# Kernel tuning notes

Measured on AMD Instinct MI355X. Metric: run time of the kernel, lower is better.

The kernel has to match this reference:

```python
import jax, jax.numpy as jnp
import numpy as np

NUM_EXPERTS = 8
TOP_K = 2
RANK = 16
LORA_ALPHA = 32
SCALING = LORA_ALPHA / RANK  # 2.0


def setup_inputs() -> dict:
    key = jax.random.key(0)
    ks = jax.random.split(key, 6)
    B, S, D_IN, D_OUT = 4, 2048, 4096, 4096
    x = jax.random.normal(ks[0], (B, S, D_IN), dtype=jnp.float32)
    W_base = jax.random.normal(ks[1], (D_OUT, D_IN), dtype=jnp.float32) * 0.02
    b_base = jax.random.normal(ks[2], (D_OUT,), dtype=jnp.float32) * 0.02
    W_router = jax.random.normal(ks[3], (NUM_EXPERTS, D_IN), dtype=jnp.float32) * 0.02
    A = jax.random.normal(ks[4], (NUM_EXPERTS, RANK, D_IN), dtype=jnp.float32) * 0.02
    Bm = jax.random.normal(ks[5], (D_OUT, RANK), dtype=jnp.float32) * 0.02
    Bm = jnp.broadcast_to(Bm, (NUM_EXPERTS, D_OUT, RANK)) * jnp.arange(1, NUM_EXPERTS + 1, dtype=jnp.float32)[:, None, None] * 0.2
    return {"x": x, "W_base": W_base, "b_base": b_base, "W_router": W_router, "A": A, "B": Bm}


def reference(x, W_base, b_base, W_router, A, B):
    bs, seq, d_in = x.shape
    T = bs * seq
    xf = x.reshape(T, d_in)  # flatten tokens, as in torch .view(-1, d_in)

    # base linear layer
    base = xf @ W_base.T + b_base  # [T, d_out]

    # local router: logits -> top-k -> softmax over selected weights
    logits = xf @ W_router.T                      # [T, E]
    rw, sel = jax.lax.top_k(logits, TOP_K)        # [T, K] each
    rw = jax.nn.softmax(rw, axis=-1)              # router_norm == 'softmax'

    # per-token per-expert combine weight (zero for unselected experts);
    # mathematically identical to gather-LoRA-scatter since top-k experts
    # per token are distinct.
    onehot = jax.nn.one_hot(sel, NUM_EXPERTS, dtype=rw.dtype)  # [T, K, E]
    w = jnp.einsum('tk,tke->te', rw, onehot)                   # [T, E]

    # LoRA: down-project to tiny rank, weight, then up-project; contract
    # expert+rank together to avoid a [T, E, d_out] intermediate.
    h = jnp.einsum('td,erd->ter', xf, A)          # [T, E, r] (small)
    lora = jnp.einsum('ter,te,eor->to', h, w, B) * SCALING  # [T, d_out]

    return (base + lora).reshape(bs, seq, -1)
```

## Files before the change

### kernel.cpp

```cpp
#include <hip/hip_runtime.h>
#include <hip/hip_bf16.h>
#include <stdint.h>

#define T_TOKENS 8192
#define DIN      4096
#define DOUT     4096
#define NE       8
#define RANK     16
#define KEXT     128
#define KTOT     4224
#define SCALING  2.0f

typedef __attribute__((ext_vector_type(8))) short   short8;
typedef __attribute__((ext_vector_type(4))) float   float4v;

__device__ __forceinline__ unsigned short f2bf(float f) {
    union { float f; unsigned int u; } c; c.f = f;
    unsigned int u = c.u;
    u += 0x7FFFu + ((u >> 16) & 1u);
    return (unsigned short)(u >> 16);
}

#define GLD_LDS(g, l) __builtin_amdgcn_global_load_lds( \
    (const __attribute__((address_space(1))) void*)(g), \
    (__attribute__((address_space(3))) void*)(l), 16, 0, 0)

__global__ __launch_bounds__(256) void k_prep_w(const float* __restrict__ Wb,
                                                unsigned short* __restrict__ Wa) {
    int idx = blockIdx.x * 256 + threadIdx.x;
    const float4* W4 = (const float4*)Wb;
    float4 v = W4[idx];
    int o  = idx >> 10;
    int kc = idx & 1023;
    ushort4 p;
    p.x = f2bf(v.x); p.y = f2bf(v.y); p.z = f2bf(v.z); p.w = f2bf(v.w);
    *(ushort4*)(Wa + (size_t)o * KTOT + kc * 4) = p;
}

__global__ __launch_bounds__(256) void k_prep_small(const float* __restrict__ A,
                                                    const float* __restrict__ Bm,
                                                    unsigned short* __restrict__ Acat,
                                                    unsigned short* __restrict__ Wa) {
    int tid = blockIdx.x * 256 + threadIdx.x;
    if (tid < NE * RANK * DIN) {
        Acat[tid] = f2bf(A[tid]);
    } else {
        int j   = tid - NE * RANK * DIN;
        int o   = j >> 7;
        int rem = j & 127;
        int e   = rem >> 4;
        int r   = rem & 15;
        Wa[(size_t)o * KTOT + DIN + rem] = f2bf(Bm[(size_t)e * (DOUT * RANK) + o * RANK + r]);
    }
}

__global__ __launch_bounds__(256) void k_router(const float* __restrict__ x,
                                                const float* __restrict__ Wr,
                                                unsigned short* __restrict__ xa,
                                                float* __restrict__ w8) {
    int t   = blockIdx.x;
    int tid = threadIdx.x;
    const float4* x4  = (const float4*)(x + (size_t)t * DIN);
    const float4* Wr4 = (const float4*)Wr;
    unsigned short* xrow = xa + (size_t)t * KTOT;

    float p[NE];
#pragma unroll
    for (int e = 0; e < NE; e++) p[e] = 0.f;

#pragma unroll
    for (int j = 0; j < 4; j++) {
        int c = tid + j * 256;
        float4 v = x4[c];
        ushort4 b;
        b.x = f2bf(v.x); b.y = f2bf(v.y); b.z = f2bf(v.z); b.w = f2bf(v.w);
        *(ushort4*)(xrow + c * 4) = b;
#pragma unroll
        for (int e = 0; e < NE; e++) {
            float4 wv = Wr4[e * 1024 + c];
            p[e] += v.x * wv.x + v.y * wv.y + v.z * wv.z + v.w * wv.w;
        }
    }
#pragma unroll
    for (int e = 0; e < NE; e++) {
        float v = p[e];
#pragma unroll
        for (int off = 32; off > 0; off >>= 1) v += __shfl_xor(v, off);
        p[e] = v;
    }
    __shared__ float red[4][NE];
    int lane = tid & 63, w = tid >> 6;
    if (lane == 0) {
#pragma unroll
        for (int e = 0; e < NE; e++) red[w][e] = p[e];
    }
    __syncthreads();
    if (tid == 0) {
        float lg[NE];
#pragma unroll
        for (int e = 0; e < NE; e++)
            lg[e] = red[0][e] + red[1][e] + red[2][e] + red[3][e];
        int e0 = 0;
#pragma unroll
        for (int e = 1; e < NE; e++) if (lg[e] > lg[e0]) e0 = e;
        int e1 = -1;
#pragma unroll
        for (int e = 0; e < NE; e++)
            if (e != e0 && (e1 < 0 || lg[e] > lg[e1])) e1 = e;
        float a0 = 1.0f;
        float a1 = __expf(lg[e1] - lg[e0]);
        float inv = 1.0f / (a0 + a1);
        float s0 = a0 * inv * SCALING;
        float s1 = a1 * inv * SCALING;
        float* wrow = w8 + t * NE;
#pragma unroll
        for (int e = 0; e < NE; e++)
            wrow[e] = (e == e0) ? s0 : ((e == e1) ? s1 : 0.f);
    }
}

__global__ __launch_bounds__(256) void k_h(unsigned short* xa,
                                           const unsigned short* __restrict__ Acat,
                                           const float* __restrict__ w8) {
    __shared__ unsigned short lds[32 * 32 + 128 * 32];
    int m0  = blockIdx.x * 32;
    int tid = threadIdx.x;
    int l = tid & 63, w = tid >> 6;
    int quad = l >> 4, lr = l & 15;

    float4v acc[2][2] = {};

    for (int k0 = 0; k0 < DIN; k0 += 32) {
        __syncthreads();
        if (w < 2) {
            int c = w * 64 + l;
            int row = c >> 2, kc = c & 3;
            GLD_LDS(xa + (size_t)(m0 + row) * KTOT + k0 + kc * 8, lds + c * 8);
        }
#pragma unroll
        for (int it = 0; it < 2; it++) {
            int c = it * 256 + w * 64 + l;
            int row = c >> 2, kc = c & 3;
            GLD_LDS(Acat + (size_t)row * DIN + k0 + kc * 8, lds + 1024 + c * 8);
        }
        __syncthreads();

        short8 a[2], b[2];
#pragma unroll
        for (int mi = 0; mi < 2; mi++)
            a[mi] = *(const short8*)(lds + (mi * 16 + lr) * 32 + quad * 8);
#pragma unroll
        for (int ni = 0; ni < 2; ni++)
            b[ni] = *(const short8*)(lds + 1024 + (w * 32 + ni * 16 + lr) * 32 + quad * 8);
#pragma unroll
        for (int mi = 0; mi < 2; mi++)
#pragma unroll
            for (int ni = 0; ni < 2; ni++)
                acc[mi][ni] = __builtin_amdgcn_mfma_f32_16x16x32_bf16(a[mi], b[ni], acc[mi][ni], 0, 0, 0);
    }

#pragma unroll
    for (int mi = 0; mi < 2; mi++)
#pragma unroll
        for (int ni = 0; ni < 2; ni++) {
            int col = w * 32 + ni * 16 + lr;
            int e = col >> 4;
#pragma unroll
            for (int i = 0; i < 4; i++) {
                int t = m0 + mi * 16 + quad * 4 + i;
                float v = acc[mi][ni][i] * w8[t * NE + e];
                xa[(size_t)t * KTOT + DIN + col] = f2bf(v);
            }
        }
}

__global__ __launch_bounds__(256) void k_main(const unsigned short* __restrict__ xa,
                                              const unsigned short* __restrict__ Wa,
                                              const float* __restrict__ bias,
                                              float* __restrict__ out) {
    __shared__ unsigned short lds[2 * 128 * 32];
    int bm = blockIdx.x, bn = blockIdx.y;
    int tid = threadIdx.x;
    int l = tid & 63, w = tid >> 6;
    int quad = l >> 4, lr = l & 15;
    int wm = w >> 1, wn = w & 1;

    const size_t xbase = (size_t)bm * 128 * KTOT;
    const size_t wbase = (size_t)bn * 128 * KTOT;

    float4v acc[4][4] = {};

    for (int k0 = 0; k0 < KTOT; k0 += 32) {
        __syncthreads();
#pragma unroll
        for (int it = 0; it < 2; it++) {
            int c = it * 256 + w * 64 + l;
            int row = c >> 2, kc = c & 3;
            GLD_LDS(xa + xbase + (size_t)row * KTOT + k0 + kc * 8, lds + c * 8);
            GLD_LDS(Wa + wbase + (size_t)row * KTOT + k0 + kc * 8, lds + 4096 + c * 8);
        }
        __syncthreads();

        short8 a[4], b[4];
#pragma unroll
        for (int mi = 0; mi < 4; mi++)
            a[mi] = *(const short8*)(lds + (wm * 64 + mi * 16 + lr) * 32 + quad * 8);
#pragma unroll
        for (int ni = 0; ni < 4; ni++)
            b[ni] = *(const short8*)(lds + 4096 + (wn * 64 + ni * 16 + lr) * 32 + quad * 8);
#pragma unroll
        for (int mi = 0; mi < 4; mi++)
#pragma unroll
            for (int ni = 0; ni < 4; ni++)
                acc[mi][ni] = __builtin_amdgcn_mfma_f32_16x16x32_bf16(a[mi], b[ni], acc[mi][ni], 0, 0, 0);
    }

    int trow0 = bm * 128 + wm * 64;
    int ocol0 = bn * 128 + wn * 64;
#pragma unroll
    for (int ni = 0; ni < 4; ni++) {
        int o = ocol0 + ni * 16 + lr;
        float bb = bias[o];
#pragma unroll
        for (int mi = 0; mi < 4; mi++) {
#pragma unroll
            for (int i = 0; i < 4; i++) {
                int t = trow0 + mi * 16 + quad * 4 + i;
                out[(size_t)t * DOUT + o] = acc[mi][ni][i] + bb;
            }
        }
    }
}

extern "C" void kernel_launch(void* const* d_in, const int* in_sizes, int n_in,
                              void* d_out, int out_size, void* d_ws, size_t ws_size,
                              hipStream_t stream) {
    const float* x  = (const float*)d_in[0];
    const float* Wb = (const float*)d_in[1];
    const float* bb = (const float*)d_in[2];
    const float* Wr = (const float*)d_in[3];
    const float* A  = (const float*)d_in[4];
    const float* Bm = (const float*)d_in[5];
    float* out = (float*)d_out;

    char* ws = (char*)d_ws;
    unsigned short* xa   = (unsigned short*)(ws);
    unsigned short* Wa   = (unsigned short*)(ws + 69206016);
    unsigned short* Acat = (unsigned short*)(ws + 69206016 + 34603008);
    float*          w8   = (float*)(ws + 69206016 + 34603008 + 1048576);

    k_prep_w    <<<dim3(16384), dim3(256), 0, stream>>>(Wb, Wa);
    k_prep_small<<<dim3(4096),  dim3(256), 0, stream>>>(A, Bm, Acat, Wa);
    k_router    <<<dim3(8192),  dim3(256), 0, stream>>>(x, Wr, xa, w8);
    k_h         <<<dim3(256),   dim3(256), 0, stream>>>(xa, Acat, w8);
    k_main      <<<dim3(64, 32), dim3(256), 0, stream>>>(xa, Wa, bb, out);
}
```

Before: 707.9 us.

## Fuse router and LoRA down-projection, merge prep kernels, swizzle LDS in main GEMM

Merges the two weight-prep kernels into one launch. Fuses the router logits, x bf16 conversion and the LoRA down-projection into a single 256-block kernel that converts each x row once and reuses it from LDS, instead of re-reading bf16 x from global memory. Adds an XOR swizzle to the LDS layout in the main GEMM and the fused kernel to reduce bank conflicts on the MFMA operand loads. The fused front kernel launches only 256 blocks, so the large fp32 x read is spread over fewer workgroups, which may lower bandwidth utilisation compared with the former 8192-block router.

```diff
diff --git a/kernel.cpp b/kernel.cpp
--- a/kernel.cpp
+++ b/kernel.cpp
@@ -25,81 +25,131 @@
     (const __attribute__((address_space(1))) void*)(g), \
     (__attribute__((address_space(3))) void*)(l), 16, 0, 0)
 
-__global__ __launch_bounds__(256) void k_prep_w(const float* __restrict__ Wb,
-                                                unsigned short* __restrict__ Wa) {
-    int idx = blockIdx.x * 256 + threadIdx.x;
-    const float4* W4 = (const float4*)Wb;
-    float4 v = W4[idx];
-    int o  = idx >> 10;
-    int kc = idx & 1023;
-    ushort4 p;
-    p.x = f2bf(v.x); p.y = f2bf(v.y); p.z = f2bf(v.z); p.w = f2bf(v.w);
-    *(ushort4*)(Wa + (size_t)o * KTOT + kc * 4) = p;
-}
-
-__global__ __launch_bounds__(256) void k_prep_small(const float* __restrict__ A,
-                                                    const float* __restrict__ Bm,
-                                                    unsigned short* __restrict__ Acat,
-                                                    unsigned short* __restrict__ Wa) {
-    int tid = blockIdx.x * 256 + threadIdx.x;
-    if (tid < NE * RANK * DIN) {
-        Acat[tid] = f2bf(A[tid]);
+__global__ __launch_bounds__(256) void k_prep(const float* __restrict__ Wb,
+                                              const float* __restrict__ A,
+                                              const float* __restrict__ Bm,
+                                              unsigned short* __restrict__ Wa,
+                                              unsigned short* __restrict__ Acat) {
+    int b = blockIdx.x;
+    if (b < 16384) {
+        int idx = b * 256 + threadIdx.x;
+        const float4* W4 = (const float4*)Wb;
+        float4 v = W4[idx];
+        int o  = idx >> 10;
+        int kc = idx & 1023;
+        ushort4 p;
+        p.x = f2bf(v.x); p.y = f2bf(v.y); p.z = f2bf(v.z); p.w = f2bf(v.w);
+        *(ushort4*)(Wa + (size_t)o * KTOT + kc * 4) = p;
     } else {
-        int j   = tid - NE * RANK * DIN;
-        int o   = j >> 7;
-        int rem = j & 127;
-        int e   = rem >> 4;
-        int r   = rem & 15;
-        Wa[(size_t)o * KTOT + DIN + rem] = f2bf(Bm[(size_t)e * (DOUT * RANK) + o * RANK + r]);
-    }
-}
-
-__global__ __launch_bounds__(256) void k_router(const float* __restrict__ x,
-                                                const float* __restrict__ Wr,
-                                                unsigned short* __restrict__ xa,
-                                                float* __restrict__ w8) {
-    int t   = blockIdx.x;
+        int tid = (b - 16384) * 256 + threadIdx.x;
+        if (tid < NE * RANK * DIN) {
+            Acat[tid] = f2bf(A[tid]);
+        } else {
+            int j   = tid - NE * RANK * DIN;
+            int o   = j >> 7;
+            int rem = j & 127;
+            int e   = rem >> 4;
+            int r   = rem & 15;
+            Wa[(size_t)o * KTOT + DIN + rem] = f2bf(Bm[(size_t)e * (DOUT * RANK) + o * RANK + r]);
+        }
+    }
+}
+
+#define FBM 32
+#define FBK 128
+__global__ __launch_bounds__(256) void k_front(const float* __restrict__ x,
+                                               const float* __restrict__ Wr,
+                                               const unsigned short* __restrict__ Acat,
+                                               unsigned short* __restrict__ xa) {
+    __shared__ unsigned short lds_x[FBM * 136];
+    __shared__ unsigned short lds_a[128 * FBK];
+    __shared__ float lds_wr[NE * FBK];
+    __shared__ float lds_red[FBM][8][NE];
+    __shared__ float lds_wsc[FBM][NE];
+
+    int m0  = blockIdx.x * FBM;
     int tid = threadIdx.x;
-    const float4* x4  = (const float4*)(x + (size_t)t * DIN);
-    const float4* Wr4 = (const float4*)Wr;
-    unsigned short* xrow = xa + (size_t)t * KTOT;
-
-    float p[NE];
-#pragma unroll
-    for (int e = 0; e < NE; e++) p[e] = 0.f;
-
-#pragma unroll
-    for (int j = 0; j < 4; j++) {
-        int c = tid + j * 256;
-        float4 v = x4[c];
-        ushort4 b;
-        b.x = f2bf(v.x); b.y = f2bf(v.y); b.z = f2bf(v.z); b.w = f2bf(v.w);
-        *(ushort4*)(xrow + c * 4) = b;
+    int t_local = tid >> 3;
+    int slice   = tid & 7;
+    int l = tid & 63, w = tid >> 6;
+    int quad = l >> 4, lr = l & 15;
+
+    const float* xrow = x + (size_t)(m0 + t_local) * DIN;
+    unsigned short* xarow = xa + (size_t)(m0 + t_local) * KTOT;
+
+    float racc[NE];
+#pragma unroll
+    for (int e = 0; e < NE; e++) racc[e] = 0.f;
+    float4v acc[2][2] = {};
+
+    for (int k0 = 0; k0 < DIN; k0 += FBK) {
+        __syncthreads();
+        float4 xv[4];
+#pragma unroll
+        for (int j = 0; j < 4; j++)
+            xv[j] = *(const float4*)(xrow + k0 + slice * 16 + j * 4);
+        short8 pk0, pk1;
+        pk0[0] = f2bf(xv[0].x); pk0[1] = f2bf(xv[0].y); pk0[2] = f2bf(xv[0].z); pk0[3] = f2bf(xv[0].w);
+        pk0[4] = f2bf(xv[1].x); pk0[5] = f2bf(xv[1].y); pk0[6] = f2bf(xv[1].z); pk0[7] = f2bf(xv[1].w);
+        pk1[0] = f2bf(xv[2].x); pk1[1] = f2bf(xv[2].y); pk1[2] = f2bf(xv[2].z); pk1[3] = f2bf(xv[2].w);
+        pk1[4] = f2bf(xv[3].x); pk1[5] = f2bf(xv[3].y); pk1[6] = f2bf(xv[3].z); pk1[7] = f2bf(xv[3].w);
+        *(short8*)(xarow + k0 + slice * 16)     = pk0;
+        *(short8*)(xarow + k0 + slice * 16 + 8) = pk1;
+        *(short8*)&lds_x[t_local * 136 + slice * 16]     = pk0;
+        *(short8*)&lds_x[t_local * 136 + slice * 16 + 8] = pk1;
+        {
+            int e = tid >> 5;
+            int c = (tid & 31) * 4;
+            *(float4*)&lds_wr[e * FBK + c] = *(const float4*)(Wr + (size_t)e * DIN + k0 + c);
+        }
+#pragma unroll
+        for (int it = 0; it < 8; it++) {
+            int c = it * 256 + tid;
+            int row = c >> 4, kc = c & 15;
+            int p = (row ^ (row >> 2)) & 15;
+            GLD_LDS(Acat + (size_t)row * DIN + k0 + (kc ^ p) * 8, lds_a + c * 8);
+        }
+        __syncthreads();
 #pragma unroll
         for (int e = 0; e < NE; e++) {
-            float4 wv = Wr4[e * 1024 + c];
-            p[e] += v.x * wv.x + v.y * wv.y + v.z * wv.z + v.w * wv.w;
-        }
-    }
-#pragma unroll
-    for (int e = 0; e < NE; e++) {
-        float v = p[e];
-#pragma unroll
-        for (int off = 32; off > 0; off >>= 1) v += __shfl_xor(v, off);
-        p[e] = v;
-    }
-    __shared__ float red[4][NE];
-    int lane = tid & 63, w = tid >> 6;
-    if (lane == 0) {
-#pragma unroll
-        for (int e = 0; e < NE; e++) red[w][e] = p[e];
-    }
+#pragma unroll
+            for (int j = 0; j < 4; j++) {
+                float4 wv = *(const float4*)&lds_wr[e * FBK + slice * 16 + j * 4];
+                racc[e] += xv[j].x * wv.x + xv[j].y * wv.y + xv[j].z * wv.z + xv[j].w * wv.w;
+            }
+        }
+#pragma unroll
+        for (int kk = 0; kk < 4; kk++) {
+            short8 a[2], b[2];
+#pragma unroll
+            for (int mi = 0; mi < 2; mi++)
+                a[mi] = *(const short8*)&lds_x[(mi * 16 + lr) * 136 + kk * 32 + quad * 8];
+#pragma unroll
+            for (int ni = 0; ni < 2; ni++) {
+                int rown = w * 32 + ni * 16 + lr;
+                int pn = (rown ^ (rown >> 2)) & 15;
+                b[ni] = *(const short8*)&lds_a[rown * FBK + ((kk * 4 + quad) ^ pn) * 8];
+            }
+#pragma unroll
+            for (int mi = 0; mi < 2; mi++)
+#pragma unroll
+                for (int ni = 0; ni < 2; ni++)
+                    acc[mi][ni] = __builtin_amdgcn_mfma_f32_16x16x32_bf16(a[mi], b[ni], acc[mi][ni], 0, 0, 0);
+        }
+    }
+
+#pragma unroll
+    for (int e = 0; e < NE; e++) lds_red[t_local][slice][e] = racc[e];
     __syncthreads();
-    if (tid == 0) {
+    if (tid < FBM) {
         float lg[NE];
 #pragma unroll
-        for (int e = 0; e < NE; e++)
-            lg[e] = red[0][e] + red[1][e] + red[2][e] + red[3][e];
+        for (int e = 0; e < NE; e++) {
+            float s = 0.f;
+#pragma unroll
+            for (int j = 0; j < 8; j++) s += lds_red[tid][j][e];
+            lg[e] = s;
+        }
         int e0 = 0;
 #pragma unroll
         for (int e = 1; e < NE; e++) if (lg[e] > lg[e0]) e0 = e;
@@ -107,57 +157,13 @@
 #pragma unroll
         for (int e = 0; e < NE; e++)
             if (e != e0 && (e1 < 0 || lg[e] > lg[e1])) e1 = e;
-        float a0 = 1.0f;
         float a1 = __expf(lg[e1] - lg[e0]);
-        float inv = 1.0f / (a0 + a1);
-        float s0 = a0 * inv * SCALING;
-        float s1 = a1 * inv * SCALING;
-        float* wrow = w8 + t * NE;
+        float inv = 1.0f / (1.0f + a1);
 #pragma unroll
         for (int e = 0; e < NE; e++)
-            wrow[e] = (e == e0) ? s0 : ((e == e1) ? s1 : 0.f);
-    }
-}
-
-__global__ __launch_bounds__(256) void k_h(unsigned short* xa,
-                                           const unsigned short* __restrict__ Acat,
-                                           const float* __restrict__ w8) {
-    __shared__ unsigned short lds[32 * 32 + 128 * 32];
-    int m0  = blockIdx.x * 32;
-    int tid = threadIdx.x;
-    int l = tid & 63, w = tid >> 6;
-    int quad = l >> 4, lr = l & 15;
-
-    float4v acc[2][2] = {};
-
-    for (int k0 = 0; k0 < DIN; k0 += 32) {
-        __syncthreads();
-        if (w < 2) {
-            int c = w * 64 + l;
-            int row = c >> 2, kc = c & 3;
-            GLD_LDS(xa + (size_t)(m0 + row) * KTOT + k0 + kc * 8, lds + c * 8);
-        }
-#pragma unroll
-        for (int it = 0; it < 2; it++) {
-            int c = it * 256 + w * 64 + l;
-            int row = c >> 2, kc = c & 3;
-            GLD_LDS(Acat + (size_t)row * DIN + k0 + kc * 8, lds + 1024 + c * 8);
-        }
-        __syncthreads();
-
-        short8 a[2], b[2];
-#pragma unroll
-        for (int mi = 0; mi < 2; mi++)
-            a[mi] = *(const short8*)(lds + (mi * 16 + lr) * 32 + quad * 8);
-#pragma unroll
-        for (int ni = 0; ni < 2; ni++)
-            b[ni] = *(const short8*)(lds + 1024 + (w * 32 + ni * 16 + lr) * 32 + quad * 8);
-#pragma unroll
-        for (int mi = 0; mi < 2; mi++)
-#pragma unroll
-            for (int ni = 0; ni < 2; ni++)
-                acc[mi][ni] = __builtin_amdgcn_mfma_f32_16x16x32_bf16(a[mi], b[ni], acc[mi][ni], 0, 0, 0);
-    }
+            lds_wsc[tid][e] = (e == e0) ? inv * SCALING : ((e == e1) ? a1 * inv * SCALING : 0.f);
+    }
+    __syncthreads();
 
 #pragma unroll
     for (int mi = 0; mi < 2; mi++)
@@ -167,9 +173,9 @@
             int e = col >> 4;
 #pragma unroll
             for (int i = 0; i < 4; i++) {
-                int t = m0 + mi * 16 + quad * 4 + i;
-                float v = acc[mi][ni][i] * w8[t * NE + e];
-                xa[(size_t)t * KTOT + DIN + col] = f2bf(v);
+                int t = mi * 16 + quad * 4 + i;
+                float v = acc[mi][ni][i] * lds_wsc[t][e];
+                xa[(size_t)(m0 + t) * KTOT + DIN + col] = f2bf(v);
             }
         }
 }
@@ -188,26 +194,31 @@
     const size_t xbase = (size_t)bm * 128 * KTOT;
     const size_t wbase = (size_t)bn * 128 * KTOT;
 
+    int pa = (lr ^ (lr >> 2)) & 3;
+    int sa = (quad ^ pa) * 8;
+
     float4v acc[4][4] = {};
 
     for (int k0 = 0; k0 < KTOT; k0 += 32) {
         __syncthreads();
 #pragma unroll
         for (int it = 0; it < 2; it++) {
-            int c = it * 256 + w * 64 + l;
+            int c = it * 256 + tid;
             int row = c >> 2, kc = c & 3;
-            GLD_LDS(xa + xbase + (size_t)row * KTOT + k0 + kc * 8, lds + c * 8);
-            GLD_LDS(Wa + wbase + (size_t)row * KTOT + k0 + kc * 8, lds + 4096 + c * 8);
+            int p = (row ^ (row >> 2)) & 3;
+            int kcs = kc ^ p;
+            GLD_LDS(xa + xbase + (size_t)row * KTOT + k0 + kcs * 8, lds + c * 8);
+            GLD_LDS(Wa + wbase + (size_t)row * KTOT + k0 + kcs * 8, lds + 4096 + c * 8);
         }
         __syncthreads();
 
         short8 a[4], b[4];
 #pragma unroll
         for (int mi = 0; mi < 4; mi++)
-            a[mi] = *(const short8*)(lds + (wm * 64 + mi * 16 + lr) * 32 + quad * 8);
+            a[mi] = *(const short8*)(lds + (wm * 64 + mi * 16 + lr) * 32 + sa);
 #pragma unroll
         for (int ni = 0; ni < 4; ni++)
-            b[ni] = *(const short8*)(lds + 4096 + (wn * 64 + ni * 16 + lr) * 32 + quad * 8);
+            b[ni] = *(const short8*)(lds + 4096 + (wn * 64 + ni * 16 + lr) * 32 + sa);
 #pragma unroll
         for (int mi = 0; mi < 4; mi++)
 #pragma unroll
@@ -247,11 +258,8 @@
     unsigned short* xa   = (unsigned short*)(ws);
     unsigned short* Wa   = (unsigned short*)(ws + 69206016);
     unsigned short* Acat = (unsigned short*)(ws + 69206016 + 34603008);
-    float*          w8   = (float*)(ws + 69206016 + 34603008 + 1048576);
-
-    k_prep_w    <<<dim3(16384), dim3(256), 0, stream>>>(Wb, Wa);
-    k_prep_small<<<dim3(4096),  dim3(256), 0, stream>>>(A, Bm, Acat, Wa);
-    k_router    <<<dim3(8192),  dim3(256), 0, stream>>>(x, Wr, xa, w8);
-    k_h         <<<dim3(256),   dim3(256), 0, stream>>>(xa, Acat, w8);
-    k_main      <<<dim3(64, 32), dim3(256), 0, stream>>>(xa, Wa, bb, out);
-}
+
+    k_prep <<<dim3(20480), dim3(256), 0, stream>>>(Wb, A, Bm, Wa, Acat);
+    k_front<<<dim3(256),   dim3(256), 0, stream>>>(x, Wr, Acat, xa);
+    k_main <<<dim3(64, 32), dim3(256), 0, stream>>>(xa, Wa, bb, out);
+}
```

Measured after the change: 667.8 us. 1.06x faster.

## Fuse prep and router kernels into one launch; deepen k_h K tile with XOR swizzle

Applied to the files above, without the earlier changes.

Merges the weight conversion, LoRA weight prep and router kernels into a single block-indexed front kernel. The router now handles one token per wavefront and stages router weights in shared memory, which removes the cross-wave reduction and cuts repeated global reads of the router weights. The k_h down-projection kernel loads 128-wide K tiles with an XOR swizzle, so it needs fewer barriers and has fewer LDS bank conflicts. In exchange, k_front uses 32KB of LDS per block on every path, which may lower occupancy for the conversion blocks that do not need it.

```diff
diff --git a/kernel.cpp b/kernel.cpp
--- a/kernel.cpp
+++ b/kernel.cpp
@@ -25,104 +25,109 @@
     (const __attribute__((address_space(1))) void*)(g), \
     (__attribute__((address_space(3))) void*)(l), 16, 0, 0)
 
-__global__ __launch_bounds__(256) void k_prep_w(const float* __restrict__ Wb,
-                                                unsigned short* __restrict__ Wa) {
-    int idx = blockIdx.x * 256 + threadIdx.x;
-    const float4* W4 = (const float4*)Wb;
-    float4 v = W4[idx];
-    int o  = idx >> 10;
-    int kc = idx & 1023;
-    ushort4 p;
-    p.x = f2bf(v.x); p.y = f2bf(v.y); p.z = f2bf(v.z); p.w = f2bf(v.w);
-    *(ushort4*)(Wa + (size_t)o * KTOT + kc * 4) = p;
-}
-
-__global__ __launch_bounds__(256) void k_prep_small(const float* __restrict__ A,
-                                                    const float* __restrict__ Bm,
-                                                    unsigned short* __restrict__ Acat,
-                                                    unsigned short* __restrict__ Wa) {
-    int tid = blockIdx.x * 256 + threadIdx.x;
-    if (tid < NE * RANK * DIN) {
-        Acat[tid] = f2bf(A[tid]);
+__global__ __launch_bounds__(256) void k_front(const float* __restrict__ x,
+                                               const float* __restrict__ Wr,
+                                               const float* __restrict__ Wb,
+                                               const float* __restrict__ A,
+                                               const float* __restrict__ Bm,
+                                               unsigned short* __restrict__ xa,
+                                               unsigned short* __restrict__ Wa,
+                                               unsigned short* __restrict__ Acat,
+                                               float* __restrict__ w8) {
+    __shared__ float lds_wr[8 * 1024];
+    int b = blockIdx.x;
+    int tid = threadIdx.x;
+
+    if (b < 2048) {
+        int l = tid & 63, w = tid >> 6;
+        int t = b * 4 + w;
+        const float4* x4 = (const float4*)x;
+        const float4* Wr4 = (const float4*)Wr;
+        unsigned short* xarow = xa + (size_t)t * KTOT;
+
+        float racc[NE];
+#pragma unroll
+        for (int e = 0; e < NE; e++) racc[e] = 0.f;
+
+        for (int ci = 0; ci < 4; ci++) {
+            __syncthreads();
+#pragma unroll
+            for (int jj = 0; jj < 8; jj++) {
+                int f = jj * 256 + tid;
+                int e = f >> 8, col = f & 255;
+                *(float4*)&lds_wr[f * 4] = Wr4[e * 1024 + ci * 256 + col];
+            }
+            __syncthreads();
+            float4 xv[4];
+#pragma unroll
+            for (int j = 0; j < 4; j++)
+                xv[j] = x4[(size_t)t * 1024 + ci * 256 + j * 64 + l];
+#pragma unroll
+            for (int j = 0; j < 4; j++) {
+                ushort4 p;
+                p.x = f2bf(xv[j].x); p.y = f2bf(xv[j].y);
+                p.z = f2bf(xv[j].z); p.w = f2bf(xv[j].w);
+                *(ushort4*)(xarow + (ci * 256 + j * 64 + l) * 4) = p;
+            }
+#pragma unroll
+            for (int e = 0; e < NE; e++) {
+#pragma unroll
+                for (int j = 0; j < 4; j++) {
+                    float4 wv = *(const float4*)&lds_wr[(e * 256 + j * 64 + l) * 4];
+                    racc[e] += xv[j].x * wv.x + xv[j].y * wv.y + xv[j].z * wv.z + xv[j].w * wv.w;
+                }
+            }
+        }
+#pragma unroll
+        for (int e = 0; e < NE; e++) {
+            float v = racc[e];
+#pragma unroll
+            for (int off = 32; off > 0; off >>= 1) v += __shfl_xor(v, off);
+            racc[e] = v;
+        }
+        if (l == 0) {
+            int e0 = 0;
+#pragma unroll
+            for (int e = 1; e < NE; e++) if (racc[e] > racc[e0]) e0 = e;
+            int e1 = -1;
+#pragma unroll
+            for (int e = 0; e < NE; e++)
+                if (e != e0 && (e1 < 0 || racc[e] > racc[e1])) e1 = e;
+            float a1 = __expf(racc[e1] - racc[e0]);
+            float inv = 1.0f / (1.0f + a1);
+            float* wrow = w8 + t * NE;
+#pragma unroll
+            for (int e = 0; e < NE; e++)
+                wrow[e] = (e == e0) ? inv * SCALING : ((e == e1) ? a1 * inv * SCALING : 0.f);
+        }
+    } else if (b < 18432) {
+        int idx = (b - 2048) * 256 + tid;
+        float4 v = ((const float4*)Wb)[idx];
+        int o  = idx >> 10;
+        int kc = idx & 1023;
+        ushort4 p;
+        p.x = f2bf(v.x); p.y = f2bf(v.y); p.z = f2bf(v.z); p.w = f2bf(v.w);
+        *(ushort4*)(Wa + (size_t)o * KTOT + kc * 4) = p;
     } else {
-        int j   = tid - NE * RANK * DIN;
-        int o   = j >> 7;
-        int rem = j & 127;
-        int e   = rem >> 4;
-        int r   = rem & 15;
-        Wa[(size_t)o * KTOT + DIN + rem] = f2bf(Bm[(size_t)e * (DOUT * RANK) + o * RANK + r]);
-    }
-}
-
-__global__ __launch_bounds__(256) void k_router(const float* __restrict__ x,
-                                                const float* __restrict__ Wr,
-                                                unsigned short* __restrict__ xa,
-                                                float* __restrict__ w8) {
-    int t   = blockIdx.x;
-    int tid = threadIdx.x;
-    const float4* x4  = (const float4*)(x + (size_t)t * DIN);
-    const float4* Wr4 = (const float4*)Wr;
-    unsigned short* xrow = xa + (size_t)t * KTOT;
-
-    float p[NE];
-#pragma unroll
-    for (int e = 0; e < NE; e++) p[e] = 0.f;
-
-#pragma unroll
-    for (int j = 0; j < 4; j++) {
-        int c = tid + j * 256;
-        float4 v = x4[c];
-        ushort4 b;
-        b.x = f2bf(v.x); b.y = f2bf(v.y); b.z = f2bf(v.z); b.w = f2bf(v.w);
-        *(ushort4*)(xrow + c * 4) = b;
-#pragma unroll
-        for (int e = 0; e < NE; e++) {
-            float4 wv = Wr4[e * 1024 + c];
-            p[e] += v.x * wv.x + v.y * wv.y + v.z * wv.z + v.w * wv.w;
-        }
-    }
-#pragma unroll
-    for (int e = 0; e < NE; e++) {
-        float v = p[e];
-#pragma unroll
-        for (int off = 32; off > 0; off >>= 1) v += __shfl_xor(v, off);
-        p[e] = v;
-    }
-    __shared__ float red[4][NE];
-    int lane = tid & 63, w = tid >> 6;
-    if (lane == 0) {
-#pragma unroll
-        for (int e = 0; e < NE; e++) red[w][e] = p[e];
-    }
-    __syncthreads();
-    if (tid == 0) {
-        float lg[NE];
-#pragma unroll
-        for (int e = 0; e < NE; e++)
-            lg[e] = red[0][e] + red[1][e] + red[2][e] + red[3][e];
-        int e0 = 0;
-#pragma unroll
-        for (int e = 1; e < NE; e++) if (lg[e] > lg[e0]) e0 = e;
-        int e1 = -1;
-#pragma unroll
-        for (int e = 0; e < NE; e++)
-            if (e != e0 && (e1 < 0 || lg[e] > lg[e1])) e1 = e;
-        float a0 = 1.0f;
-        float a1 = __expf(lg[e1] - lg[e0]);
-        float inv = 1.0f / (a0 + a1);
-        float s0 = a0 * inv * SCALING;
-        float s1 = a1 * inv * SCALING;
-        float* wrow = w8 + t * NE;
-#pragma unroll
-        for (int e = 0; e < NE; e++)
-            wrow[e] = (e == e0) ? s0 : ((e == e1) ? s1 : 0.f);
-    }
-}
-
-__global__ __launch_bounds__(256) void k_h(unsigned short* xa,
+        int tid2 = (b - 18432) * 256 + tid;
+        if (tid2 < NE * RANK * DIN) {
+            Acat[tid2] = f2bf(A[tid2]);
+        } else {
+            int j   = tid2 - NE * RANK * DIN;
+            int o   = j >> 7;
+            int rem = j & 127;
+            int e   = rem >> 4;
+            int r   = rem & 15;
+            Wa[(size_t)o * KTOT + DIN + rem] = f2bf(Bm[(size_t)e * (DOUT * RANK) + o * RANK + r]);
+        }
+    }
+}
+
+__global__ __launch_bounds__(256) void k_h(unsigned short* __restrict__ xa,
                                            const unsigned short* __restrict__ Acat,
                                            const float* __restrict__ w8) {
-    __shared__ unsigned short lds[32 * 32 + 128 * 32];
+    __shared__ unsigned short lds_x[32 * 128];
+    __shared__ unsigned short lds_a[128 * 128];
     int m0  = blockIdx.x * 32;
     int tid = threadIdx.x;
     int l = tid & 63, w = tid >> 6;
@@ -130,33 +135,43 @@
 
     float4v acc[2][2] = {};
 
-    for (int k0 = 0; k0 < DIN; k0 += 32) {
-        __syncthreads();
-        if (w < 2) {
-            int c = w * 64 + l;
-            int row = c >> 2, kc = c & 3;
-            GLD_LDS(xa + (size_t)(m0 + row) * KTOT + k0 + kc * 8, lds + c * 8);
-        }
+    for (int k0 = 0; k0 < DIN; k0 += 128) {
+        __syncthreads();
 #pragma unroll
         for (int it = 0; it < 2; it++) {
-            int c = it * 256 + w * 64 + l;
-            int row = c >> 2, kc = c & 3;
-            GLD_LDS(Acat + (size_t)row * DIN + k0 + kc * 8, lds + 1024 + c * 8);
-        }
-        __syncthreads();
-
-        short8 a[2], b[2];
-#pragma unroll
-        for (int mi = 0; mi < 2; mi++)
-            a[mi] = *(const short8*)(lds + (mi * 16 + lr) * 32 + quad * 8);
-#pragma unroll
-        for (int ni = 0; ni < 2; ni++)
-            b[ni] = *(const short8*)(lds + 1024 + (w * 32 + ni * 16 + lr) * 32 + quad * 8);
-#pragma unroll
-        for (int mi = 0; mi < 2; mi++)
-#pragma unroll
-            for (int ni = 0; ni < 2; ni++)
-                acc[mi][ni] = __builtin_amdgcn_mfma_f32_16x16x32_bf16(a[mi], b[ni], acc[mi][ni], 0, 0, 0);
+            int c = it * 256 + tid;
+            int row = c >> 4, s = c & 15;
+            int kc = s ^ (row & 15);
+            GLD_LDS(xa + (size_t)(m0 + row) * KTOT + k0 + kc * 8, lds_x + c * 8);
+        }
+#pragma unroll
+        for (int it = 0; it < 8; it++) {
+            int c = it * 256 + tid;
+            int row = c >> 4, s = c & 15;
+            int kc = s ^ (row & 15);
+            GLD_LDS(Acat + (size_t)row * DIN + k0 + kc * 8, lds_a + c * 8);
+        }
+        __syncthreads();
+#pragma unroll
+        for (int kk = 0; kk < 4; kk++) {
+            int kc = kk * 4 + quad;
+            short8 a[2], bfr[2];
+#pragma unroll
+            for (int mi = 0; mi < 2; mi++) {
+                int row = mi * 16 + lr;
+                a[mi] = *(const short8*)&lds_x[row * 128 + ((kc ^ lr) * 8)];
+            }
+#pragma unroll
+            for (int ni = 0; ni < 2; ni++) {
+                int row = w * 32 + ni * 16 + lr;
+                bfr[ni] = *(const short8*)&lds_a[row * 128 + ((kc ^ lr) * 8)];
+            }
+#pragma unroll
+            for (int mi = 0; mi < 2; mi++)
+#pragma unroll
+                for (int ni = 0; ni < 2; ni++)
+                    acc[mi][ni] = __builtin_amdgcn_mfma_f32_16x16x32_bf16(a[mi], bfr[ni], acc[mi][ni], 0, 0, 0);
+        }
     }
 
 #pragma unroll
@@ -194,7 +209,7 @@
         __syncthreads();
 #pragma unroll
         for (int it = 0; it < 2; it++) {
-            int c = it * 256 + w * 64 + l;
+            int c = it * 256 + tid;
             int row = c >> 2, kc = c & 3;
             GLD_LDS(xa + xbase + (size_t)row * KTOT + k0 + kc * 8, lds + c * 8);
             GLD_LDS(Wa + wbase + (size_t)row * KTOT + k0 + kc * 8, lds + 4096 + c * 8);
@@ -249,9 +264,7 @@
     unsigned short* Acat = (unsigned short*)(ws + 69206016 + 34603008);
     float*          w8   = (float*)(ws + 69206016 + 34603008 + 1048576);
 
-    k_prep_w    <<<dim3(16384), dim3(256), 0, stream>>>(Wb, Wa);
-    k_prep_small<<<dim3(4096),  dim3(256), 0, stream>>>(A, Bm, Acat, Wa);
-    k_router    <<<dim3(8192),  dim3(256), 0, stream>>>(x, Wr, xa, w8);
-    k_h         <<<dim3(256),   dim3(256), 0, stream>>>(xa, Acat, w8);
-    k_main      <<<dim3(64, 32), dim3(256), 0, stream>>>(xa, Wa, bb, out);
-}
+    k_front<<<dim3(22528), dim3(256), 0, stream>>>(x, Wr, Wb, A, Bm, xa, Wa, Acat, w8);
+    k_h    <<<dim3(256),   dim3(256), 0, stream>>>(xa, Acat, w8);
+    k_main <<<dim3(64, 32), dim3(256), 0, stream>>>(xa, Wa, bb, out);
+}
```

Measured after the change: 629.1 us. 11.1% less time.
